# Optimization experiments

Hardware: AMD Instinct MI355X
Metric: run time of the kernel (lower is better)

## Reference

```python
import jax, jax.numpy as jnp
import numpy as np

B, D = 4, 128          # batch, spatial grid size
N = 160000
CIN, COUT, K = 32, 32, 27
EPS = 1e-5             # torch BatchNorm1d default
SLOPE = 0.01           # torch LeakyReLU default


def _build_sparse_topology():
    """Random unique active voxel coords + 27-neighbor indice pairs (-1 = missing)."""
    rng = np.random.default_rng(0)
    total = B * D * D * D
    lin = np.sort(rng.choice(total, size=N, replace=False)).astype(np.int64)
    b = lin // (D * D * D)
    rem = lin % (D * D * D)
    z, y, x = rem // (D * D), (rem // D) % D, rem % D
    lut = np.full(total, -1, np.int32)
    lut[lin] = np.arange(N, dtype=np.int32)
    nbr = np.full((N, K), -1, np.int32)
    k = 0
    for dz in (-1, 0, 1):
        for dy in (-1, 0, 1):
            for dx in (-1, 0, 1):
                zz, yy, xx = z + dz, y + dy, x + dx
                valid = (zz >= 0) & (zz < D) & (yy >= 0) & (yy < D) & (xx >= 0) & (xx < D)
                nl = ((b * D + zz) * D + yy) * D + xx
                nbr[valid, k] = lut[nl[valid]]
                k += 1
    return nbr


def setup_inputs() -> dict:
    key = jax.random.key(0)
    kf, kw, kb = jax.random.split(key, 3)
    neighbor_idx = jnp.asarray(_build_sparse_topology())
    features = jax.random.normal(kf, (N, CIN), dtype=jnp.float32)
    w_scale = 1.0 / np.sqrt(K * CIN)
    weight = jax.random.normal(kw, (K, CIN, COUT), dtype=jnp.float32) * w_scale
    bias = jax.random.normal(kb, (COUT,), dtype=jnp.float32) * 0.01
    gamma = jnp.ones((COUT,), dtype=jnp.float32)
    beta = jnp.zeros((COUT,), dtype=jnp.float32)
    return {"features": features, "neighbor_idx": neighbor_idx, "weight": weight,
            "bias": bias, "gamma": gamma, "beta": beta}


def reference(features, neighbor_idx, weight, bias, gamma, beta):
    # --- submanifold 3x3x3 sparse conv: gather -> per-offset GEMM -> accumulate ---
    mask = (neighbor_idx >= 0)                       # [N,27]
    idx = jnp.maximum(neighbor_idx, 0)
    gathered = features[idx] * mask[..., None].astype(features.dtype)  # [N,27,Cin]
    out = jnp.einsum('nkc,kcd->nd', gathered, weight) + bias           # [N,Cout]
    # --- BatchNorm1d (training-mode batch stats, biased variance) ---
    mean = jnp.mean(out, axis=0)
    var = jnp.var(out, axis=0)
    out = (out - mean) * jax.lax.rsqrt(var + EPS) * gamma + beta
    # --- LeakyReLU ---
    return jnp.where(out >= 0, out, SLOPE * out)
```

## Files before the change

kernel.cpp:

```cpp
#include <hip/hip_runtime.h>

#define NVOX  160000
#define KOFF  27
#define EPSV  1e-5f
#define SLOPE 0.01f
#define NBLK  2500
#define PADP  2560

using bf16x8 = __attribute__((ext_vector_type(8))) __bf16;
using f32x4  = __attribute__((ext_vector_type(4))) float;
using i32x4  = __attribute__((ext_vector_type(4))) int;
using u16    = unsigned short;
typedef __attribute__((ext_vector_type(4), aligned(4))) int i32x4u;
typedef __attribute__((ext_vector_type(2), aligned(4))) int i32x2u;


__global__ void pack_weights(const float* __restrict__ w, u16* __restrict__ wp) {
    int tid = blockIdx.x * blockDim.x + threadIdx.x;
    if (tid >= KOFF * 2 * 64 * 8) return;
    int j = tid & 7;
    int L = (tid >> 3) & 63;
    int f = (tid >> 9) & 1;
    int k = tid >> 10;
    int c = ((L >> 4) << 3) + j;
    int d = (f << 4) + (L & 15);
    __bf16 b = (__bf16)w[(k * 32 + c) * 32 + d];
    wp[tid] = __builtin_bit_cast(u16, b);
}

__global__ __launch_bounds__(256) void conv_f32(
    const float* __restrict__ feat,
    const int*  __restrict__ nbr,
    const i32x4* __restrict__ wp,
    float* __restrict__ out,
    float* __restrict__ partials)
{
    const int lane  = threadIdx.x & 63;
    const int wid   = (blockIdx.x * 256 + threadIdx.x) >> 6;
    const int vbase = wid * 16;
    const int m = lane & 15;
    const int q = lane >> 4;

    const int* row = nbr + (size_t)(vbase + m) * KOFF;
    int id[27];
    *(i32x4u*)(id +  0) = *(const i32x4u*)(row +  0);
    *(i32x4u*)(id +  4) = *(const i32x4u*)(row +  4);
    *(i32x4u*)(id +  8) = *(const i32x4u*)(row +  8);
    *(i32x4u*)(id + 12) = *(const i32x4u*)(row + 12);
    *(i32x4u*)(id + 16) = *(const i32x4u*)(row + 16);
    *(i32x4u*)(id + 20) = *(const i32x4u*)(row + 20);
    *(i32x2u*)(id + 24) = *(const i32x2u*)(row + 24);
    id[26] = row[26];

    f32x4 acc0 = {}, acc1 = {};

#pragma unroll
    for (int b = 0; b < 3; ++b) {
        f32x4 lo[9], hi[9];
#pragma unroll
        for (int j = 0; j < 9; ++j) {
            int k = b * 9 + j;
            if (__ballot(id[k] >= 0)) {
                int v_id = id[k];
                int safe = v_id >= 0 ? v_id : 0;
                const f32x4* fp = (const f32x4*)(feat + (size_t)safe * 32 + q * 8);
                lo[j] = fp[0];
                hi[j] = fp[1];
            }
        }
#pragma unroll
        for (int j = 0; j < 9; ++j) {
            int k = b * 9 + j;
            if (__ballot(id[k] >= 0)) {
                bf16x8 t;
#pragma unroll
                for (int jj = 0; jj < 4; ++jj) {
                    t[jj]     = (__bf16)lo[j][jj];
                    t[4 + jj] = (__bf16)hi[j][jj];
                }
                bf16x8 z = {};
                bf16x8 a = (id[k] < 0) ? z : t;
                i32x4 b0r = wp[(k * 2 + 0) * 64 + lane];
                i32x4 b1r = wp[(k * 2 + 1) * 64 + lane];
                bf16x8 b0 = __builtin_bit_cast(bf16x8, b0r);
                bf16x8 b1 = __builtin_bit_cast(bf16x8, b1r);
                acc0 = __builtin_amdgcn_mfma_f32_16x16x32_bf16(a, b0, acc0, 0, 0, 0);
                acc1 = __builtin_amdgcn_mfma_f32_16x16x32_bf16(a, b1, acc1, 0, 0, 0);
            }
        }
    }

    float s0 = 0, s1 = 0, sq0 = 0, sq1 = 0;
#pragma unroll
    for (int r = 0; r < 4; ++r) {
        int v = vbase + q * 4 + r;
        float x0 = acc0[r], x1 = acc1[r];
        s0 += x0; sq0 += x0 * x0;
        s1 += x1; sq1 += x1 * x1;
        out[v * 32 + m]      = x0;
        out[v * 32 + 16 + m] = x1;
    }
    s0  += __shfl_xor(s0, 16, 64);  s0  += __shfl_xor(s0, 32, 64);
    s1  += __shfl_xor(s1, 16, 64);  s1  += __shfl_xor(s1, 32, 64);
    sq0 += __shfl_xor(sq0, 16, 64); sq0 += __shfl_xor(sq0, 32, 64);
    sq1 += __shfl_xor(sq1, 16, 64); sq1 += __shfl_xor(sq1, 32, 64);

    __shared__ float red[4][64];
    int w = threadIdx.x >> 6;
    if (lane < 16) {
        red[w][m]      = s0;
        red[w][16 + m] = s1;
        red[w][32 + m] = sq0;
        red[w][48 + m] = sq1;
    }
    __syncthreads();
    if (threadIdx.x < 64) {
        int t = threadIdx.x;
        partials[(size_t)t * PADP + blockIdx.x] =
            red[0][t] + red[1][t] + red[2][t] + red[3][t];
    }
}

__global__ __launch_bounds__(256) void reduce_stats(
    const float* __restrict__ partials, float* __restrict__ stats)
{
    const float* prow = partials + (size_t)blockIdx.x * PADP;
    float s = 0.f;
    for (int p = threadIdx.x; p < NBLK; p += 256) s += prow[p];
#pragma unroll
    for (int off = 1; off < 64; off <<= 1) s += __shfl_xor(s, off, 64);
    __shared__ float sd[4];
    int lane = threadIdx.x & 63, w = threadIdx.x >> 6;
    if (lane == 0) sd[w] = s;
    __syncthreads();
    if (threadIdx.x == 0) stats[blockIdx.x] = sd[0] + sd[1] + sd[2] + sd[3];
}

__global__ __launch_bounds__(256) void apply_bn(
    f32x4* __restrict__ o, const float* __restrict__ stats,
    const float* __restrict__ gamma, const float* __restrict__ beta)
{
    __shared__ float s[64];
    int t = threadIdx.x;
    if (t < 32) {
        float mean = stats[t] * (1.f / NVOX);
        float var  = stats[32 + t] * (1.f / NVOX) - mean * mean;
        float rstd = rsqrtf(var + EPSV);
        float scale = gamma[t] * rstd;
        s[t]      = scale;
        s[32 + t] = beta[t] - mean * scale;
    }
    __syncthreads();
    int i = blockIdx.x * 256 + t;
#pragma unroll
    for (int rep = 0; rep < 2; ++rep) {
        int i2 = i * 2 + rep;
        f32x4 v = o[i2];
        int c0 = (i2 & 7) * 4;
        f32x4 r;
#pragma unroll
        for (int j = 0; j < 4; ++j) {
            float y = v[j] * s[c0 + j] + s[32 + c0 + j];
            r[j] = (y >= 0.f) ? y : SLOPE * y;
        }
        o[i2] = r;
    }
}

extern "C" void kernel_launch(void* const* d_in, const int* in_sizes, int n_in,
                              void* d_out, int out_size, void* d_ws, size_t ws_size,
                              hipStream_t stream) {
    const float* feat  = (const float*)d_in[0];
    const int*   nbr   = (const int*)d_in[1];
    const float* w     = (const float*)d_in[2];
    const float* gamma = (const float*)d_in[4];
    const float* beta  = (const float*)d_in[5];

    char* ws = (char*)d_ws;
    float* partials = (float*)ws;
    u16*   wp       = (u16*)(ws + 655360);
    float* stats    = (float*)(ws + 655360 + 55296);

    pack_weights<<<108, 256, 0, stream>>>(w, wp);
    conv_f32<<<NBLK, 256, 0, stream>>>(feat, nbr, (const i32x4*)wp,
                                       (float*)d_out, partials);
    reduce_stats<<<64, 256, 0, stream>>>(partials, stats);
    apply_bn<<<2500, 256, 0, stream>>>((f32x4*)d_out, stats, gamma, beta);
}
```

Measured before the change: 123.3 us.

## Split kernel offsets across waves per 16-voxel tile with LDS reduction

```diff
diff --git a/kernel.cpp b/kernel.cpp
--- a/kernel.cpp
+++ b/kernel.cpp
@@ -4,20 +4,20 @@
 #define KOFF  27
 #define EPSV  1e-5f
 #define SLOPE 0.01f
-#define NBLK  2500
-#define PADP  2560
+#define CBLK  10000
+#define WPELE (KOFF * 2 * 64 * 8)
 
 using bf16x8 = __attribute__((ext_vector_type(8))) __bf16;
 using f32x4  = __attribute__((ext_vector_type(4))) float;
+using f32x2  = __attribute__((ext_vector_type(2))) float;
 using i32x4  = __attribute__((ext_vector_type(4))) int;
 using u16    = unsigned short;
 typedef __attribute__((ext_vector_type(4), aligned(4))) int i32x4u;
-typedef __attribute__((ext_vector_type(2), aligned(4))) int i32x2u;
 
 
 __global__ void pack_weights(const float* __restrict__ w, u16* __restrict__ wp) {
     int tid = blockIdx.x * blockDim.x + threadIdx.x;
-    if (tid >= KOFF * 2 * 64 * 8) return;
+    if (tid >= WPELE) return;
     int j = tid & 7;
     int L = (tid >> 3) & 63;
     int f = (tid >> 9) & 1;
@@ -28,112 +28,99 @@
     wp[tid] = __builtin_bit_cast(u16, b);
 }
 
-__global__ __launch_bounds__(256) void conv_f32(
+__global__ __launch_bounds__(256) void conv_mfma(
     const float* __restrict__ feat,
     const int*  __restrict__ nbr,
     const i32x4* __restrict__ wp,
     float* __restrict__ out,
     float* __restrict__ partials)
 {
-    const int lane  = threadIdx.x & 63;
-    const int wid   = (blockIdx.x * 256 + threadIdx.x) >> 6;
-    const int vbase = wid * 16;
-    const int m = lane & 15;
-    const int q = lane >> 4;
+    __shared__ float pacc[4 * 512];
+    __shared__ float ssum[32], ssq[32];
 
+    const int t    = threadIdx.x;
+    const int w    = t >> 6;
+    const int lane = t & 63;
+    const int m    = lane & 15;
+    const int q    = lane >> 4;
+    const int tile = blockIdx.x;
+    const int vbase = tile * 16;
+
+    if (t < 32) { ssum[t] = 0.f; ssq[t] = 0.f; }
+
+    const int k0 = w * 7;
     const int* row = nbr + (size_t)(vbase + m) * KOFF;
-    int id[27];
-    *(i32x4u*)(id +  0) = *(const i32x4u*)(row +  0);
-    *(i32x4u*)(id +  4) = *(const i32x4u*)(row +  4);
-    *(i32x4u*)(id +  8) = *(const i32x4u*)(row +  8);
-    *(i32x4u*)(id + 12) = *(const i32x4u*)(row + 12);
-    *(i32x4u*)(id + 16) = *(const i32x4u*)(row + 16);
-    *(i32x4u*)(id + 20) = *(const i32x4u*)(row + 20);
-    *(i32x2u*)(id + 24) = *(const i32x2u*)(row + 24);
-    id[26] = row[26];
+    i32x4 a4 = *(const i32x4u*)(row + k0);
+    i32x4 b4 = *(const i32x4u*)(row + k0 + (w == 3 ? 2 : 3));
+    int id[7];
+    id[0] = a4[0]; id[1] = a4[1]; id[2] = a4[2]; id[3] = a4[3];
+    if (w == 3) { id[4] = b4[2]; id[5] = b4[3]; id[6] = -1; }
+    else        { id[4] = b4[1]; id[5] = b4[2]; id[6] = b4[3]; }
 
     f32x4 acc0 = {}, acc1 = {};
 
 #pragma unroll
-    for (int b = 0; b < 3; ++b) {
-        f32x4 lo[9], hi[9];
+    for (int j = 0; j < 7; ++j) {
+        if (__ballot(id[j] >= 0)) {
+            int v_id = id[j];
+            int safe = v_id >= 0 ? v_id : 0;
+            const f32x4* fp = (const f32x4*)(feat + (size_t)safe * 32 + q * 8);
+            f32x4 lo = fp[0], hi = fp[1];
+            bf16x8 tv;
 #pragma unroll
-        for (int j = 0; j < 9; ++j) {
-            int k = b * 9 + j;
-            if (__ballot(id[k] >= 0)) {
-                int v_id = id[k];
-                int safe = v_id >= 0 ? v_id : 0;
-                const f32x4* fp = (const f32x4*)(feat + (size_t)safe * 32 + q * 8);
-                lo[j] = fp[0];
-                hi[j] = fp[1];
+            for (int jj = 0; jj < 4; ++jj) {
+                tv[jj]     = (__bf16)lo[jj];
+                tv[4 + jj] = (__bf16)hi[jj];
             }
-        }
-#pragma unroll
-        for (int j = 0; j < 9; ++j) {
-            int k = b * 9 + j;
-            if (__ballot(id[k] >= 0)) {
-                bf16x8 t;
-#pragma unroll
-                for (int jj = 0; jj < 4; ++jj) {
-                    t[jj]     = (__bf16)lo[j][jj];
-                    t[4 + jj] = (__bf16)hi[j][jj];
-                }
-                bf16x8 z = {};
-                bf16x8 a = (id[k] < 0) ? z : t;
-                i32x4 b0r = wp[(k * 2 + 0) * 64 + lane];
-                i32x4 b1r = wp[(k * 2 + 1) * 64 + lane];
-                bf16x8 b0 = __builtin_bit_cast(bf16x8, b0r);
-                bf16x8 b1 = __builtin_bit_cast(bf16x8, b1r);
-                acc0 = __builtin_amdgcn_mfma_f32_16x16x32_bf16(a, b0, acc0, 0, 0, 0);
-                acc1 = __builtin_amdgcn_mfma_f32_16x16x32_bf16(a, b1, acc1, 0, 0, 0);
-            }
+            bf16x8 z = {};
+            bf16x8 a = (v_id < 0) ? z : tv;
+            int k = k0 + j;
+            i32x4 b0r = wp[(k * 2 + 0) * 64 + lane];
+            i32x4 b1r = wp[(k * 2 + 1) * 64 + lane];
+            bf16x8 b0 = __builtin_bit_cast(bf16x8, b0r);
+            bf16x8 b1 = __builtin_bit_cast(bf16x8, b1r);
+            acc0 = __builtin_amdgcn_mfma_f32_16x16x32_bf16(a, b0, acc0, 0, 0, 0);
+            acc1 = __builtin_amdgcn_mfma_f32_16x16x32_bf16(a, b1, acc1, 0, 0, 0);
         }
     }
 
-    float s0 = 0, s1 = 0, sq0 = 0, sq1 = 0;
 #pragma unroll
     for (int r = 0; r < 4; ++r) {
-        int v = vbase + q * 4 + r;
-        float x0 = acc0[r], x1 = acc1[r];
-        s0 += x0; sq0 += x0 * x0;
-        s1 += x1; sq1 += x1 * x1;
-        out[v * 32 + m]      = x0;
-        out[v * 32 + 16 + m] = x1;
-    }
-    s0  += __shfl_xor(s0, 16, 64);  s0  += __shfl_xor(s0, 32, 64);
-    s1  += __shfl_xor(s1, 16, 64);  s1  += __shfl_xor(s1, 32, 64);
-    sq0 += __shfl_xor(sq0, 16, 64); sq0 += __shfl_xor(sq0, 32, 64);
-    sq1 += __shfl_xor(sq1, 16, 64); sq1 += __shfl_xor(sq1, 32, 64);
-
-    __shared__ float red[4][64];
-    int w = threadIdx.x >> 6;
-    if (lane < 16) {
-        red[w][m]      = s0;
-        red[w][16 + m] = s1;
-        red[w][32 + m] = sq0;
-        red[w][48 + m] = sq1;
+        int vox = q * 4 + r;
+        pacc[w * 512 + vox * 32 + m]      = acc0[r];
+        pacc[w * 512 + vox * 32 + 16 + m] = acc1[r];
     }
     __syncthreads();
-    if (threadIdx.x < 64) {
-        int t = threadIdx.x;
-        partials[(size_t)t * PADP + blockIdx.x] =
-            red[0][t] + red[1][t] + red[2][t] + red[3][t];
-    }
+
+    int e0 = t * 2;
+    float f0 = pacc[e0]     + pacc[512 + e0]     + pacc[1024 + e0]     + pacc[1536 + e0];
+    float f1 = pacc[e0 + 1] + pacc[512 + e0 + 1] + pacc[1024 + e0 + 1] + pacc[1536 + e0 + 1];
+    f32x2 st = {f0, f1};
+    *(f32x2*)(out + (size_t)vbase * 32 + e0) = st;
+
+    atomicAdd(&ssum[e0 & 31], f0);
+    atomicAdd(&ssq [e0 & 31], f0 * f0);
+    atomicAdd(&ssum[(e0 + 1) & 31], f1);
+    atomicAdd(&ssq [(e0 + 1) & 31], f1 * f1);
+    __syncthreads();
+
+    if (t < 64)
+        partials[(size_t)tile * 64 + t] = (t < 32) ? ssum[t] : ssq[t - 32];
 }
 
 __global__ __launch_bounds__(256) void reduce_stats(
     const float* __restrict__ partials, float* __restrict__ stats)
 {
-    const float* prow = partials + (size_t)blockIdx.x * PADP;
+    int c = blockIdx.x;
     float s = 0.f;
-    for (int p = threadIdx.x; p < NBLK; p += 256) s += prow[p];
+    for (int p = threadIdx.x; p < CBLK; p += 256) s += partials[(size_t)p * 64 + c];
 #pragma unroll
     for (int off = 1; off < 64; off <<= 1) s += __shfl_xor(s, off, 64);
     __shared__ float sd[4];
     int lane = threadIdx.x & 63, w = threadIdx.x >> 6;
     if (lane == 0) sd[w] = s;
     __syncthreads();
-    if (threadIdx.x == 0) stats[blockIdx.x] = sd[0] + sd[1] + sd[2] + sd[3];
+    if (threadIdx.x == 0) stats[c] = sd[0] + sd[1] + sd[2] + sd[3];
 }
 
 __global__ __launch_bounds__(256) void apply_bn(
@@ -177,13 +164,13 @@
     const float* beta  = (const float*)d_in[5];
 
     char* ws = (char*)d_ws;
-    float* partials = (float*)ws;
-    u16*   wp       = (u16*)(ws + 655360);
-    float* stats    = (float*)(ws + 655360 + 55296);
+    u16*   wp       = (u16*)ws;
+    float* partials = (float*)(ws + 55296);
+    float* stats    = (float*)(ws + 55296 + 2560000);
 
     pack_weights<<<108, 256, 0, stream>>>(w, wp);
-    conv_f32<<<NBLK, 256, 0, stream>>>(feat, nbr, (const i32x4*)wp,
-                                       (float*)d_out, partials);
+    conv_mfma<<<CBLK, 256, 0, stream>>>(feat, nbr, (const i32x4*)wp,
+                                        (float*)d_out, partials);
     reduce_stats<<<64, 256, 0, stream>>>(partials, stats);
     apply_bn<<<2500, 256, 0, stream>>>((f32x4*)d_out, stats, gamma, beta);
 }
```

Result: slower. 165.6 us (+34.3%).
